# Performance work log

Hardware: AMD Instinct MI355X
Metric: run time of the kernel (lower is better)

The kernel has to match this reference:

```python
import jax, jax.numpy as jnp
import numpy as np

B, S, D = 1, 2048, 1024
H, HD = 16, 64          # attention heads, head dim (kv_heads = 1 -> MQA)
E, K, FH = 8, 2, 4096   # experts, top-k, expert hidden dim
EPS = 1e-5


def setup_inputs() -> dict:
    key = jax.random.key(0)
    ks = jax.random.split(key, 8)
    std = 0.02
    return {
        "x": jax.random.normal(ks[0], (B, S, D), jnp.float32),
        "Wq": jax.random.normal(ks[1], (D, H * HD), jnp.float32) * std,
        "Wk": jax.random.normal(ks[2], (D, HD), jnp.float32) * std,   # 1 kv head
        "Wv": jax.random.normal(ks[3], (D, HD), jnp.float32) * std,
        "Wo": jax.random.normal(ks[4], (H * HD, D), jnp.float32) * std,
        "g_pre_mqa": jnp.ones((D,), jnp.float32),
        "g_post_mqa": jnp.ones((D,), jnp.float32),
        "g_pre_moe": jnp.ones((D,), jnp.float32),
        "g_post_moe": jnp.ones((D,), jnp.float32),
        "Wr": jax.random.normal(ks[5], (D, E), jnp.float32) * std,
        "W1": jax.random.normal(ks[6], (E, D, FH), jnp.float32) * std,
        "W2": jax.random.normal(ks[7], (E, FH, D), jnp.float32) * std,
    }


def rmsnorm(x, g):
    return x * jax.lax.rsqrt(jnp.mean(x * x, axis=-1, keepdims=True) + EPS) * g


def reference(x, Wq, Wk, Wv, Wo, g_pre_mqa, g_post_mqa, g_pre_moe, g_post_moe, Wr, W1, W2):
    # --- MQA block (inference path, no dropout, no causal mask in source) ---
    h = rmsnorm(x, g_pre_mqa)
    q = (h @ Wq).reshape(B, S, H, HD)
    k = h @ Wk  # [B,S,HD] single kv head, broadcast over H
    v = h @ Wv
    scores = jnp.einsum('bqhd,bkd->bhqk', q, k) / np.float32(np.sqrt(HD))
    probs_attn = jax.nn.softmax(scores, axis=-1)
    attn = jnp.einsum('bhqk,bkd->bqhd', probs_attn, v).reshape(B, S, H * HD) @ Wo
    x = x + rmsnorm(attn, g_post_mqa)

    # --- MoE block: softmax router, top-k sparse combine ---
    h = rmsnorm(x, g_pre_moe)
    logits = h @ Wr                                # [B,S,E]
    routing_probs = jax.nn.softmax(logits, axis=-1)
    _, top_idx = jax.lax.top_k(routing_probs, K)   # [B,S,K]
    mask = jax.nn.one_hot(top_idx, E, dtype=routing_probs.dtype).sum(axis=-2)
    weights = routing_probs * mask                 # zero non-chosen experts
    hid = jax.nn.gelu(jnp.einsum('bsd,edf->bsef', h, W1))   # [B,S,E,FH]
    eout = jnp.einsum('bsef,efd->bsed', hid, W2)            # [B,S,E,D]
    moe_out = jnp.einsum('bsed,bse->bsd', eout, weights)
    x = x + rmsnorm(moe_out, g_post_moe)
    return x, routing_probs
```

## Files before the change

kernel.cpp:

```cpp
#include <hip/hip_runtime.h>

typedef unsigned short u16;

#define DEVFN static __device__ __forceinline__

constexpr int Sq = 2048, Dm = 1024, NH = 16, HDim = 64, NE = 8, FHid = 4096;

typedef __attribute__((ext_vector_type(8))) short bf16x8;
typedef __attribute__((ext_vector_type(4))) float f32x4;

DEVFN float b2f(u16 u) { return __uint_as_float(((unsigned)u) << 16); }
DEVFN u16 f2b(float f) {
  unsigned u = __float_as_uint(f);
  return (u16)((u + 0x7fffu + ((u >> 16) & 1u)) >> 16);
}
DEVFN float gelu_f(float x) {
  float y = 0.7978845608028654f * (x + 0.044715f * x * x * x);
  float t = 1.0f - 2.0f / (__expf(2.0f * y) + 1.0f);
  return 0.5f * x * (1.0f + t);
}

DEVFN void gload16(const u16* g, u16* l) {
  __builtin_amdgcn_global_load_lds((const __attribute__((address_space(1))) void*)g,
                                   (__attribute__((address_space(3))) void*)l, 16, 0, 0);
}

__global__ __launch_bounds__(256) void detect_k(const u16* __restrict__ x, int* __restrict__ flag) {
  int t = threadIdx.x;
  float mx = 0.f;
  for (int i = t; i < 4096; i += 256) mx = fmaxf(mx, fabsf(b2f(x[i])));
#pragma unroll
  for (int m = 32; m; m >>= 1) mx = fmaxf(mx, __shfl_xor(mx, m, 64));
  __shared__ float red[4];
  if ((t & 63) == 0) red[t >> 6] = mx;
  __syncthreads();
  if (t == 0) {
    float m2 = fmaxf(fmaxf(red[0], red[1]), fmaxf(red[2], red[3]));
    flag[0] = (m2 > 1e6f) ? 1 : 0;
  }
}

template <int INM, int RESM>
__global__ __launch_bounds__(64) void rmsnorm2_k(const void* __restrict__ inp, const void* __restrict__ g,
                                                 const void* __restrict__ resp, float* __restrict__ out1,
                                                 const int* __restrict__ dflag) {
  int isf = dflag[0];
  int row = blockIdx.x, t = threadIdx.x;
  long rb = (long)row * Dm;
  float v[16];
#pragma unroll
  for (int j = 0; j < 4; j++) {
    long o = rb + t * 4 + j * 256;
    if (INM == 0 || isf) {
      float4 f = *((const float4*)((const float*)inp + o));
      v[4 * j] = f.x; v[4 * j + 1] = f.y; v[4 * j + 2] = f.z; v[4 * j + 3] = f.w;
    } else {
      ushort4 u = *((const ushort4*)((const u16*)inp + o));
      v[4 * j] = b2f(u.x); v[4 * j + 1] = b2f(u.y); v[4 * j + 2] = b2f(u.z); v[4 * j + 3] = b2f(u.w);
    }
  }
  float ss = 0.f;
#pragma unroll
  for (int j = 0; j < 16; j++) ss += v[j] * v[j];
#pragma unroll
  for (int m = 32; m; m >>= 1) ss += __shfl_xor(ss, m, 64);
  float sc = rsqrtf(ss * (1.0f / Dm) + 1e-5f);
#pragma unroll
  for (int j = 0; j < 4; j++) {
    long o = rb + t * 4 + j * 256;
    int go = t * 4 + j * 256;
    float gf[4];
    if (isf) {
      float4 gv = *((const float4*)((const float*)g + go));
      gf[0] = gv.x; gf[1] = gv.y; gf[2] = gv.z; gf[3] = gv.w;
    } else {
      ushort4 gu = *((const ushort4*)((const u16*)g + go));
      gf[0] = b2f(gu.x); gf[1] = b2f(gu.y); gf[2] = b2f(gu.z); gf[3] = b2f(gu.w);
    }
    float o4[4];
#pragma unroll
    for (int q = 0; q < 4; q++) o4[q] = v[4 * j + q] * sc * gf[q];
    if constexpr (RESM == 1) {
      float4 rf = *((const float4*)((const float*)resp + o));
      o4[0] += rf.x; o4[1] += rf.y; o4[2] += rf.z; o4[3] += rf.w;
    } else if constexpr (RESM == 2) {
      if (isf) {
        float4 rf = *((const float4*)((const float*)resp + o));
        o4[0] += rf.x; o4[1] += rf.y; o4[2] += rf.z; o4[3] += rf.w;
      } else {
        ushort4 ru = *((const ushort4*)((const u16*)resp + o));
        o4[0] += b2f(ru.x); o4[1] += b2f(ru.y); o4[2] += b2f(ru.z); o4[3] += b2f(ru.w);
      }
    }
    float4 of;
    of.x = o4[0]; of.y = o4[1]; of.z = o4[2]; of.w = o4[3];
    *((float4*)(out1 + o)) = of;
  }
}

template <int OP>
__global__ __launch_bounds__(256) void gemm_nn_k(
    const float* __restrict__ A, const void* __restrict__ Braw, long boff,
    float* __restrict__ C, int M, int N, int K,
    const float* __restrict__ wfull, int eidx, const int* __restrict__ dflag) {
  int isf = dflag[0];
  const float* Bf = (const float*)Braw;
  const u16* Bh = (const u16*)Braw;
  int t = threadIdx.x;
  int m0 = blockIdx.y * 64, n0 = blockIdx.x * 64;

  __shared__ float As[64][20];
  __shared__ float Bs[16][68];

  int ty = t >> 4, tx = t & 15;
  float acc[4][4];
#pragma unroll
  for (int i = 0; i < 4; i++)
#pragma unroll
    for (int j = 0; j < 4; j++) acc[i][j] = 0.f;

  for (int k0 = 0; k0 < K; k0 += 16) {
    __syncthreads();
#pragma unroll
    for (int i = 0; i < 4; i++) {
      int idx = t + i * 256;
      int ar = idx >> 4, ac = idx & 15;
      As[ar][ac] = A[(long)(m0 + ar) * K + k0 + ac];
      int br = idx >> 6, bc = idx & 63;
      long bi = boff + (long)(k0 + br) * N + n0 + bc;
      Bs[br][bc] = isf ? Bf[bi] : b2f(Bh[bi]);
    }
    __syncthreads();
#pragma unroll
    for (int kk = 0; kk < 16; kk++) {
      float a[4], b[4];
#pragma unroll
      for (int i = 0; i < 4; i++) a[i] = As[ty * 4 + i][kk];
#pragma unroll
      for (int j = 0; j < 4; j++) b[j] = Bs[kk][tx * 4 + j];
#pragma unroll
      for (int i = 0; i < 4; i++)
#pragma unroll
        for (int j = 0; j < 4; j++) acc[i][j] += a[i] * b[j];
    }
  }
#pragma unroll
  for (int i = 0; i < 4; i++) {
    int row = m0 + ty * 4 + i;
#pragma unroll
    for (int j = 0; j < 4; j++) {
      int col = n0 + tx * 4 + j;
      long cidx = (long)row * N + col;
      float val = acc[i][j];
      if constexpr (OP == 0) C[cidx] = val;
      else if constexpr (OP == 1) C[cidx] = gelu_f(val);
      else C[cidx] += wfull[(long)row * 8 + eidx] * val;
    }
  }
}

__global__ __launch_bounds__(256) void attn_f32_k(
    const float* __restrict__ Qf, const float* __restrict__ Kf, const float* __restrict__ Vf,
    float* __restrict__ Of) {
  int qb = blockIdx.x, h = blockIdx.y;
  int t = threadIdx.x;
  int qr = t >> 2;
  int sub = t & 3;
  __shared__ float Ks[64][68];
  __shared__ float Vs[64][68];
  int qrow = qb * 64 + qr;
  const float* qp = Qf + (long)qrow * Dm + h * HDim + sub * 16;
  float qfr[16];
#pragma unroll
  for (int j = 0; j < 16; j += 4) {
    float4 v = *(const float4*)(qp + j);
    qfr[j] = v.x; qfr[j + 1] = v.y; qfr[j + 2] = v.z; qfr[j + 3] = v.w;
  }
  float o[16];
#pragma unroll
  for (int j = 0; j < 16; j++) o[j] = 0.f;
  float m_i = -3e38f, l_i = 0.f;

  for (int kb = 0; kb < Sq / 64; kb++) {
    __syncthreads();
#pragma unroll
    for (int i = 0; i < 2; i++) {
      int idx = t + i * 256;
      int r = idx >> 3, c8 = (idx & 7) * 8;
      const float* kp = Kf + (long)(kb * 64 + r) * HDim + c8;
      float4 a = *(const float4*)(kp);
      float4 b = *(const float4*)(kp + 4);
      *(float4*)&Ks[r][c8] = a;
      *(float4*)&Ks[r][c8 + 4] = b;
      const float* vp = Vf + (long)(kb * 64 + r) * HDim + c8;
      float4 c = *(const float4*)(vp);
      float4 d = *(const float4*)(vp + 4);
      *(float4*)&Vs[r][c8] = c;
      *(float4*)&Vs[r][c8 + 4] = d;
    }
    __syncthreads();
    float s[64];
#pragma unroll
    for (int j = 0; j < 64; j++) {
      float acc = 0.f;
#pragma unroll
      for (int d = 0; d < 16; d++) acc += qfr[d] * Ks[j][sub * 16 + d];
      s[j] = acc;
    }
#pragma unroll
    for (int j = 0; j < 64; j++) {
      float v = s[j];
      v += __shfl_xor(v, 1, 64);
      v += __shfl_xor(v, 2, 64);
      s[j] = v * 0.125f;
    }
    float mx = s[0];
#pragma unroll
    for (int j = 1; j < 64; j++) mx = fmaxf(mx, s[j]);
    float mn = fmaxf(m_i, mx);
    float alpha = __expf(m_i - mn);
    m_i = mn;
    float ps = 0.f;
#pragma unroll
    for (int j = 0; j < 64; j++) {
      s[j] = __expf(s[j] - mn);
      ps += s[j];
    }
    l_i = l_i * alpha + ps;
#pragma unroll
    for (int d = 0; d < 16; d++) o[d] *= alpha;
#pragma unroll
    for (int j = 0; j < 64; j++)
#pragma unroll
      for (int d = 0; d < 16; d++) o[d] += s[j] * Vs[j][sub * 16 + d];
  }
  float inv = 1.0f / l_i;
#pragma unroll
  for (int d = 0; d < 16; d++)
    Of[(long)qrow * Dm + h * HDim + sub * 16 + d] = o[d] * inv;
}

__global__ __launch_bounds__(256) void router2_k(const float* __restrict__ h2, const void* __restrict__ Wr,
                                                 float* __restrict__ probs_out, float* __restrict__ wfull,
                                                 const int* __restrict__ dflag,
                                                 int* __restrict__ ecnt, int* __restrict__ elist) {
  int isf = dflag[0];
  int tok = blockIdx.x * 256 + threadIdx.x;
  if (tok >= Sq) return;
  const float* hrow = h2 + (long)tok * Dm;
  float acc[8] = {0, 0, 0, 0, 0, 0, 0, 0};
  for (int i = 0; i < Dm; i++) {
    float hv = hrow[i];
    if (isf) {
      const float* wr = (const float*)Wr + (long)i * 8;
#pragma unroll
      for (int e = 0; e < 8; e++) acc[e] += hv * wr[e];
    } else {
      const u16* wr = (const u16*)Wr + (long)i * 8;
#pragma unroll
      for (int e = 0; e < 8; e++) acc[e] += hv * b2f(wr[e]);
    }
  }
  int i1 = 0;
#pragma unroll
  for (int e = 1; e < 8; e++)
    if (acc[e] > acc[i1]) i1 = e;
  int i2 = (i1 == 0) ? 1 : 0;
#pragma unroll
  for (int e = 0; e < 8; e++)
    if (e != i1 && acc[e] > acc[i2]) i2 = e;
  float mx = acc[i1];
  float pr[8], s = 0.f;
#pragma unroll
  for (int e = 0; e < 8; e++) { pr[e] = expf(acc[e] - mx); s += pr[e]; }
  float inv = 1.0f / s;
#pragma unroll
  for (int e = 0; e < 8; e++) {
    float pe = pr[e] * inv;
    probs_out[(long)tok * 8 + e] = pe;
    wfull[(long)tok * 8 + e] = (e == i1 || e == i2) ? pe : 0.f;
  }
  int p1 = atomicAdd(&ecnt[i1], 1);
  elist[i1 * Sq + p1] = tok;
  int p2 = atomicAdd(&ecnt[i2], 1);
  elist[i2 * Sq + p2] = tok;
}

__global__ __launch_bounds__(256) void split_pair_k(const float* __restrict__ in, u16* __restrict__ hi,
                                                    u16* __restrict__ lo, int n4) {
  int i = blockIdx.x * 256 + threadIdx.x;
  if (i >= n4) return;
  float4 v = ((const float4*)in)[i];
  ushort4 h, l;
  h.x = f2b(v.x); l.x = f2b(v.x - b2f(h.x));
  h.y = f2b(v.y); l.y = f2b(v.y - b2f(h.y));
  h.z = f2b(v.z); l.z = f2b(v.z - b2f(h.z));
  h.w = f2b(v.w); l.w = f2b(v.w - b2f(h.w));
  ((ushort4*)hi)[i] = h;
  ((ushort4*)lo)[i] = l;
}

__global__ __launch_bounds__(256) void transpose_bf16_k(const void* __restrict__ B, long boff,
                                                        u16* __restrict__ BT, int K, int N,
                                                        const int* __restrict__ dflag) {
  int isf = dflag[0];
  __shared__ u16 tile[32][33];
  int n0 = blockIdx.x * 32, k0 = blockIdx.y * 32;
  int tx = threadIdx.x & 31, ty = threadIdx.x >> 5;
#pragma unroll
  for (int j = 0; j < 32; j += 8) {
    long idx = boff + (long)(k0 + ty + j) * N + n0 + tx;
    u16 uv = isf ? f2b(((const float*)B)[idx]) : ((const u16*)B)[idx];
    tile[ty + j][tx] = uv;
  }
  __syncthreads();
#pragma unroll
  for (int j = 0; j < 32; j += 8)
    BT[(long)(n0 + ty + j) * K + k0 + tx] = tile[tx][ty + j];
}

__global__ __launch_bounds__(256) void moe_w1_k(
    const u16* __restrict__ Ah, const u16* __restrict__ Al, const u16* __restrict__ BT,
    u16* __restrict__ Ch, u16* __restrict__ Cl, const float* __restrict__ wfull,
    const int* __restrict__ elist, const int* __restrict__ ecnt, int eidx) {
  constexpr int N = FHid, K = Dm;
  int cnt = ecnt[eidx];
  int m0 = blockIdx.y * 128, n0 = blockIdx.x * 128;
  if (m0 >= cnt) return;
  __shared__ __align__(16) u16 sAh[128 * 32];
  __shared__ __align__(16) u16 sAl[128 * 32];
  __shared__ __align__(16) u16 sBT[128 * 32];
  __shared__ int sTok[128];
  int t = threadIdx.x;
  if (t < 128) {
    int r = m0 + t;
    sTok[t] = (r < cnt) ? elist[eidx * Sq + r] : elist[eidx * Sq];
  }
  int l = t & 63, w = t >> 6;
  int wm = w >> 1, wn = w & 1;
  int lr = l & 15, lg = l >> 4;

  f32x4 zero = {0.f, 0.f, 0.f, 0.f};
  f32x4 acc[4][4];
#pragma unroll
  for (int i = 0; i < 4; i++)
#pragma unroll
    for (int j = 0; j < 4; j++) acc[i][j] = zero;

  for (int k0 = 0; k0 < K; k0 += 32) {
    __syncthreads();
#pragma unroll
    for (int i = 0; i < 2; i++) {
      int s = i * 256 + t;
      int r = s >> 2, c = s & 3;
      long ao = (long)sTok[r] * K + k0 + c * 8;
      gload16(Ah + ao, sAh + s * 8);
      gload16(Al + ao, sAl + s * 8);
      gload16(BT + (long)(n0 + r) * K + k0 + c * 8, sBT + s * 8);
    }
    __syncthreads();
    bf16x8 fah[4], fal[4], fbb[4];
#pragma unroll
    for (int f = 0; f < 4; f++) {
      int ra = wm * 64 + f * 16 + lr;
      fah[f] = *(const bf16x8*)(sAh + ra * 32 + lg * 8);
      fal[f] = *(const bf16x8*)(sAl + ra * 32 + lg * 8);
      int rb = wn * 64 + f * 16 + lr;
      fbb[f] = *(const bf16x8*)(sBT + rb * 32 + lg * 8);
    }
#pragma unroll
    for (int i = 0; i < 4; i++)
#pragma unroll
      for (int j = 0; j < 4; j++) {
        acc[i][j] = __builtin_amdgcn_mfma_f32_16x16x32_bf16(fah[i], fbb[j], acc[i][j], 0, 0, 0);
        acc[i][j] = __builtin_amdgcn_mfma_f32_16x16x32_bf16(fal[i], fbb[j], acc[i][j], 0, 0, 0);
      }
  }

#pragma unroll
  for (int i = 0; i < 4; i++) {
#pragma unroll
    for (int j = 0; j < 4; j++) {
#pragma unroll
      for (int q = 0; q < 4; q++) {
        int widx = wm * 64 + i * 16 + lg * 4 + q;
        int col = n0 + wn * 64 + j * 16 + lr;
        bool valid = (m0 + widx) < cnt;
        int tok = sTok[widx];
        float gv = valid ? gelu_f(acc[i][j][q]) * wfull[(long)tok * 8 + eidx] : 0.f;
        u16 hh = f2b(gv);
        long idx = (long)(m0 + widx) * N + col;
        Ch[idx] = hh;
        Cl[idx] = f2b(gv - b2f(hh));
      }
    }
  }
}

__global__ __launch_bounds__(256) void moe_w2_k(
    const u16* __restrict__ Ah, const u16* __restrict__ Al, const u16* __restrict__ BT,
    float* __restrict__ C, const int* __restrict__ elist, const int* __restrict__ ecnt, int eidx) {
  constexpr int N = Dm, K = FHid;
  int cnt = ecnt[eidx];
  int m0 = blockIdx.y * 128, n0 = blockIdx.x * 128;
  if (m0 >= cnt) return;
  int kbeg = blockIdx.z * (K / 4), kend = kbeg + K / 4;
  __shared__ __align__(16) u16 sAh[128 * 32];
  __shared__ __align__(16) u16 sAl[128 * 32];
  __shared__ __align__(16) u16 sBT[128 * 32];
  __shared__ int sTok[128];
  int t = threadIdx.x;
  if (t < 128) {
    int r = m0 + t;
    sTok[t] = (r < cnt) ? elist[eidx * Sq + r] : elist[eidx * Sq];
  }
  int l = t & 63, w = t >> 6;
  int wm = w >> 1, wn = w & 1;
  int lr = l & 15, lg = l >> 4;

  f32x4 zero = {0.f, 0.f, 0.f, 0.f};
  f32x4 acc[4][4];
#pragma unroll
  for (int i = 0; i < 4; i++)
#pragma unroll
    for (int j = 0; j < 4; j++) acc[i][j] = zero;

  for (int k0 = kbeg; k0 < kend; k0 += 32) {
    __syncthreads();
#pragma unroll
    for (int i = 0; i < 2; i++) {
      int s = i * 256 + t;
      int r = s >> 2, c = s & 3;
      long ao = (long)(m0 + r) * K + k0 + c * 8;
      gload16(Ah + ao, sAh + s * 8);
      gload16(Al + ao, sAl + s * 8);
      gload16(BT + (long)(n0 + r) * K + k0 + c * 8, sBT + s * 8);
    }
    __syncthreads();
    bf16x8 fah[4], fal[4], fbb[4];
#pragma unroll
    for (int f = 0; f < 4; f++) {
      int ra = wm * 64 + f * 16 + lr;
      fah[f] = *(const bf16x8*)(sAh + ra * 32 + lg * 8);
      fal[f] = *(const bf16x8*)(sAl + ra * 32 + lg * 8);
      int rb = wn * 64 + f * 16 + lr;
      fbb[f] = *(const bf16x8*)(sBT + rb * 32 + lg * 8);
    }
#pragma unroll
    for (int i = 0; i < 4; i++)
#pragma unroll
      for (int j = 0; j < 4; j++) {
        acc[i][j] = __builtin_amdgcn_mfma_f32_16x16x32_bf16(fah[i], fbb[j], acc[i][j], 0, 0, 0);
        acc[i][j] = __builtin_amdgcn_mfma_f32_16x16x32_bf16(fal[i], fbb[j], acc[i][j], 0, 0, 0);
      }
  }

#pragma unroll
  for (int i = 0; i < 4; i++) {
#pragma unroll
    for (int j = 0; j < 4; j++) {
#pragma unroll
      for (int q = 0; q < 4; q++) {
        int widx = wm * 64 + i * 16 + lg * 4 + q;
        int col = n0 + wn * 64 + j * 16 + lr;
        if ((m0 + widx) < cnt) {
          int tok = sTok[widx];
          atomicAdd(&C[(long)tok * N + col], acc[i][j][q]);
        }
      }
    }
  }
}

extern "C" void kernel_launch(void* const* d_in, const int* in_sizes, int n_in,
                              void* d_out, int out_size, void* d_ws, size_t ws_size,
                              hipStream_t stream) {
  (void)in_sizes; (void)n_in;
  const void* x = d_in[0];
  const void* Wq = d_in[1];
  const void* Wk = d_in[2];
  const void* Wv = d_in[3];
  const void* Wo = d_in[4];
  const void* gpre = d_in[5];
  const void* gpost = d_in[6];
  const void* gpm = d_in[7];
  const void* gpo = d_in[8];
  const void* Wr = d_in[9];
  const void* W1 = d_in[10];
  const void* W2 = d_in[11];

  char* ws = (char*)d_ws;
  size_t off = 0;
  auto AL = [&](size_t b) { size_t o = off; off += (b + 255) & ~(size_t)255; return o; };
  const size_t oFlag = AL(16);
  const size_t oWf = AL((size_t)Sq * NE * 4);
  const size_t oHid = AL((size_t)Sq * FHid * 4);
  const size_t oH2 = AL((size_t)Sq * Dm * 4);
  const size_t oX2 = AL((size_t)Sq * Dm * 4);
  const size_t oMoe = AL((size_t)Sq * Dm * 4);
  const size_t oAp = AL((size_t)Sq * Dm * 4);
  const size_t oAt = AL((size_t)Sq * Dm * 4);
  const size_t oVf = AL((size_t)Sq * HDim * 4);
  const size_t oKf = AL((size_t)Sq * HDim * 4);
  const size_t oQf = AL((size_t)Sq * Dm * 4);
  const size_t oH1 = AL((size_t)Sq * Dm * 4);
  if (off > ws_size || out_size != Sq * Dm + Sq * NE) return;

  float* h1f = (float*)(ws + oH1);
  float* qf = (float*)(ws + oQf);
  float* kf = (float*)(ws + oKf);
  float* vf = (float*)(ws + oVf);
  float* attnf = (float*)(ws + oAt);
  float* attnp = (float*)(ws + oAp);
  float* x2 = (float*)(ws + oX2);
  float* h2f = (float*)(ws + oH2);
  float* moe = (float*)(ws + oMoe);
  float* wfull = (float*)(ws + oWf);
  int* dflag = (int*)(ws + oFlag);
  u16* hidh = (u16*)(ws + oHid);
  u16* hidl = hidh + (size_t)Sq * FHid;
  u16* bt1 = (u16*)(ws + oAt);
  u16* bt2 = (u16*)(ws + oAp);
  u16* h2h = (u16*)(ws + oQf);
  u16* h2l = h2h + (size_t)Sq * Dm;
  int* ecnt = (int*)(ws + oVf);
  int* elist = (int*)(ws + oVf + 256);
  float* out_x = (float*)d_out;
  float* out_probs = out_x + (size_t)Sq * Dm;

  detect_k<<<1, 256, 0, stream>>>((const u16*)x, dflag);

  rmsnorm2_k<1, 0><<<Sq, 64, 0, stream>>>(x, gpre, nullptr, h1f, dflag);

  gemm_nn_k<0><<<dim3(Dm / 64, Sq / 64), 256, 0, stream>>>(h1f, Wq, 0, qf, Sq, Dm, Dm, nullptr, 0, dflag);
  gemm_nn_k<0><<<dim3(HDim / 64, Sq / 64), 256, 0, stream>>>(h1f, Wk, 0, kf, Sq, HDim, Dm, nullptr, 0, dflag);
  gemm_nn_k<0><<<dim3(HDim / 64, Sq / 64), 256, 0, stream>>>(h1f, Wv, 0, vf, Sq, HDim, Dm, nullptr, 0, dflag);

  attn_f32_k<<<dim3(Sq / 64, NH), 256, 0, stream>>>(qf, kf, vf, attnf);

  gemm_nn_k<0><<<dim3(Dm / 64, Sq / 64), 256, 0, stream>>>(attnf, Wo, 0, attnp, Sq, Dm, Dm, nullptr, 0, dflag);

  rmsnorm2_k<0, 2><<<Sq, 64, 0, stream>>>(attnp, gpost, x, x2, dflag);
  rmsnorm2_k<0, 0><<<Sq, 64, 0, stream>>>(x2, gpm, nullptr, h2f, dflag);

  hipMemsetAsync(ws + oVf, 0, 32, stream);
  router2_k<<<Sq / 256, 256, 0, stream>>>(h2f, Wr, out_probs, wfull, dflag, ecnt, elist);

  split_pair_k<<<(Sq * Dm / 4 + 255) / 256, 256, 0, stream>>>(h2f, h2h, h2l, Sq * Dm / 4);

  hipMemsetAsync(ws + oMoe, 0, (size_t)Sq * Dm * 4, stream);
  for (int e = 0; e < NE; e++) {
    transpose_bf16_k<<<dim3(FHid / 32, Dm / 32), 256, 0, stream>>>(
        W1, (long)e * Dm * FHid, bt1, Dm, FHid, dflag);
    moe_w1_k<<<dim3(FHid / 128, Sq / 128), 256, 0, stream>>>(
        h2h, h2l, bt1, hidh, hidl, wfull, elist, ecnt, e);
    transpose_bf16_k<<<dim3(Dm / 32, FHid / 32), 256, 0, stream>>>(
        W2, (long)e * FHid * Dm, bt2, FHid, Dm, dflag);
    moe_w2_k<<<dim3(Dm / 128, Sq / 128, 4), 256, 0, stream>>>(
        hidh, hidl, bt2, moe, elist, ecnt, e);
  }

  rmsnorm2_k<0, 1><<<Sq, 64, 0, stream>>>(moe, gpo, x2, out_x, dflag);
}
```

Measured before the change: 2.488 ms.

## Retile projection GEMMs, parallelize router, merge transposes, drop atomics in expert down-proj

```diff
diff --git a/kernel.cpp b/kernel.cpp
--- a/kernel.cpp
+++ b/kernel.cpp
@@ -43,7 +43,8 @@
 template <int INM, int RESM>
 __global__ __launch_bounds__(64) void rmsnorm2_k(const void* __restrict__ inp, const void* __restrict__ g,
                                                  const void* __restrict__ resp, float* __restrict__ out1,
-                                                 const int* __restrict__ dflag) {
+                                                 const int* __restrict__ dflag,
+                                                 const void* __restrict__ inp2) {
   int isf = dflag[0];
   int row = blockIdx.x, t = threadIdx.x;
   long rb = (long)row * Dm;
@@ -51,7 +52,12 @@
 #pragma unroll
   for (int j = 0; j < 4; j++) {
     long o = rb + t * 4 + j * 256;
-    if (INM == 0 || isf) {
+    if constexpr (INM == 2) {
+      float4 f = *((const float4*)((const float*)inp + o));
+      float4 f2 = *((const float4*)((const float*)inp2 + o));
+      v[4 * j] = f.x + f2.x; v[4 * j + 1] = f.y + f2.y;
+      v[4 * j + 2] = f.z + f2.z; v[4 * j + 3] = f.w + f2.w;
+    } else if (INM == 0 || isf) {
       float4 f = *((const float4*)((const float*)inp + o));
       v[4 * j] = f.x; v[4 * j + 1] = f.y; v[4 * j + 2] = f.z; v[4 * j + 3] = f.w;
     } else {
@@ -155,6 +161,65 @@
       if constexpr (OP == 0) C[cidx] = val;
       else if constexpr (OP == 1) C[cidx] = gelu_f(val);
       else C[cidx] += wfull[(long)row * 8 + eidx] * val;
+    }
+  }
+}
+
+__global__ __launch_bounds__(256) void gemm_big_k(
+    const float* __restrict__ A, const void* __restrict__ Braw,
+    float* __restrict__ C, int M, int N, int K, const int* __restrict__ dflag) {
+  int isf = dflag[0];
+  const float* Bf = (const float*)Braw;
+  const u16* Bh = (const u16*)Braw;
+  int t = threadIdx.x;
+  int m0 = blockIdx.y * 128, n0 = blockIdx.x * 64;
+
+  __shared__ float As[128][21];
+  __shared__ float Bs[16][68];
+
+  int ty = t >> 4, tx = t & 15;
+  float acc[8][4];
+#pragma unroll
+  for (int i = 0; i < 8; i++)
+#pragma unroll
+    for (int j = 0; j < 4; j++) acc[i][j] = 0.f;
+
+  for (int k0 = 0; k0 < K; k0 += 16) {
+    __syncthreads();
+#pragma unroll
+    for (int i = 0; i < 8; i++) {
+      int idx = t + i * 256;
+      int ar = idx >> 4, ac = idx & 15;
+      As[ar][ac] = A[(long)(m0 + ar) * K + k0 + ac];
+    }
+#pragma unroll
+    for (int i = 0; i < 4; i++) {
+      int idx = t + i * 256;
+      int br = idx >> 6, bc = idx & 63;
+      long bi = (long)(k0 + br) * N + n0 + bc;
+      Bs[br][bc] = isf ? Bf[bi] : b2f(Bh[bi]);
+    }
+    __syncthreads();
+#pragma unroll
+    for (int kk = 0; kk < 16; kk++) {
+      float a[8], b[4];
+#pragma unroll
+      for (int i = 0; i < 8; i++) a[i] = As[ty * 8 + i][kk];
+#pragma unroll
+      for (int j = 0; j < 4; j++) b[j] = Bs[kk][tx * 4 + j];
+#pragma unroll
+      for (int i = 0; i < 8; i++)
+#pragma unroll
+        for (int j = 0; j < 4; j++) acc[i][j] += a[i] * b[j];
+    }
+  }
+#pragma unroll
+  for (int i = 0; i < 8; i++) {
+    int row = m0 + ty * 8 + i;
+#pragma unroll
+    for (int j = 0; j < 4; j++) {
+      int col = n0 + tx * 4 + j;
+      C[(long)row * N + col] = acc[i][j];
     }
   }
 }
@@ -245,45 +310,57 @@
                                                  const int* __restrict__ dflag,
                                                  int* __restrict__ ecnt, int* __restrict__ elist) {
   int isf = dflag[0];
-  int tok = blockIdx.x * 256 + threadIdx.x;
+  int gid = blockIdx.x * 256 + threadIdx.x;
+  int tok = gid >> 3, e = gid & 7;
   if (tok >= Sq) return;
   const float* hrow = h2 + (long)tok * Dm;
-  float acc[8] = {0, 0, 0, 0, 0, 0, 0, 0};
-  for (int i = 0; i < Dm; i++) {
-    float hv = hrow[i];
-    if (isf) {
-      const float* wr = (const float*)Wr + (long)i * 8;
-#pragma unroll
-      for (int e = 0; e < 8; e++) acc[e] += hv * wr[e];
-    } else {
-      const u16* wr = (const u16*)Wr + (long)i * 8;
-#pragma unroll
-      for (int e = 0; e < 8; e++) acc[e] += hv * b2f(wr[e]);
-    }
-  }
+  float acc = 0.f;
+  if (isf) {
+    const float* wr = (const float*)Wr;
+    for (int i = 0; i < Dm; i += 4) {
+      float4 h4 = *(const float4*)(hrow + i);
+      acc += h4.x * wr[(long)i * 8 + e];
+      acc += h4.y * wr[(long)(i + 1) * 8 + e];
+      acc += h4.z * wr[(long)(i + 2) * 8 + e];
+      acc += h4.w * wr[(long)(i + 3) * 8 + e];
+    }
+  } else {
+    const u16* wr = (const u16*)Wr;
+    for (int i = 0; i < Dm; i += 4) {
+      float4 h4 = *(const float4*)(hrow + i);
+      acc += h4.x * b2f(wr[(long)i * 8 + e]);
+      acc += h4.y * b2f(wr[(long)(i + 1) * 8 + e]);
+      acc += h4.z * b2f(wr[(long)(i + 2) * 8 + e]);
+      acc += h4.w * b2f(wr[(long)(i + 3) * 8 + e]);
+    }
+  }
+  int lane = threadIdx.x & 63;
+  int gbase = lane & ~7;
+  float vals[8];
+#pragma unroll
+  for (int e2 = 0; e2 < 8; e2++) vals[e2] = __shfl(acc, gbase + e2, 64);
   int i1 = 0;
 #pragma unroll
-  for (int e = 1; e < 8; e++)
-    if (acc[e] > acc[i1]) i1 = e;
+  for (int e2 = 1; e2 < 8; e2++)
+    if (vals[e2] > vals[i1]) i1 = e2;
   int i2 = (i1 == 0) ? 1 : 0;
 #pragma unroll
-  for (int e = 0; e < 8; e++)
-    if (e != i1 && acc[e] > acc[i2]) i2 = e;
-  float mx = acc[i1];
+  for (int e2 = 0; e2 < 8; e2++)
+    if (e2 != i1 && vals[e2] > vals[i2]) i2 = e2;
+  float mx = vals[i1];
   float pr[8], s = 0.f;
 #pragma unroll
-  for (int e = 0; e < 8; e++) { pr[e] = expf(acc[e] - mx); s += pr[e]; }
+  for (int e2 = 0; e2 < 8; e2++) { pr[e2] = expf(vals[e2] - mx); s += pr[e2]; }
   float inv = 1.0f / s;
-#pragma unroll
-  for (int e = 0; e < 8; e++) {
-    float pe = pr[e] * inv;
-    probs_out[(long)tok * 8 + e] = pe;
-    wfull[(long)tok * 8 + e] = (e == i1 || e == i2) ? pe : 0.f;
-  }
-  int p1 = atomicAdd(&ecnt[i1], 1);
-  elist[i1 * Sq + p1] = tok;
-  int p2 = atomicAdd(&ecnt[i2], 1);
-  elist[i2 * Sq + p2] = tok;
+  float pe = pr[e] * inv;
+  probs_out[(long)tok * 8 + e] = pe;
+  wfull[(long)tok * 8 + e] = (e == i1 || e == i2) ? pe : 0.f;
+  if (e == 0) {
+    int p1 = atomicAdd(&ecnt[i1], 1);
+    elist[i1 * Sq + p1] = tok;
+    int p2 = atomicAdd(&ecnt[i2], 1);
+    elist[i2 * Sq + p2] = tok;
+  }
 }
 
 __global__ __launch_bounds__(256) void split_pair_k(const float* __restrict__ in, u16* __restrict__ hi,
@@ -300,12 +377,18 @@
   ((ushort4*)lo)[i] = l;
 }
 
-__global__ __launch_bounds__(256) void transpose_bf16_k(const void* __restrict__ B, long boff,
-                                                        u16* __restrict__ BT, int K, int N,
-                                                        const int* __restrict__ dflag) {
+__global__ __launch_bounds__(256) void transpose2_k(const void* __restrict__ W1p, const void* __restrict__ W2p,
+                                                    long boff, u16* __restrict__ bt1, u16* __restrict__ bt2,
+                                                    const int* __restrict__ dflag) {
   int isf = dflag[0];
+  int z = blockIdx.z;
+  const void* B = z ? W2p : W1p;
+  u16* BT = z ? bt2 : bt1;
+  int K = z ? FHid : Dm;
+  int N = z ? Dm : FHid;
+  int n0 = blockIdx.x * 32, k0 = blockIdx.y * 32;
+  if (n0 >= N || k0 >= K) return;
   __shared__ u16 tile[32][33];
-  int n0 = blockIdx.x * 32, k0 = blockIdx.y * 32;
   int tx = threadIdx.x & 31, ty = threadIdx.x >> 5;
 #pragma unroll
   for (int j = 0; j < 32; j += 8) {
@@ -399,15 +482,17 @@
 
 __global__ __launch_bounds__(256) void moe_w2_k(
     const u16* __restrict__ Ah, const u16* __restrict__ Al, const u16* __restrict__ BT,
-    float* __restrict__ C, const int* __restrict__ elist, const int* __restrict__ ecnt, int eidx) {
+    float* __restrict__ C0, float* __restrict__ C1,
+    const int* __restrict__ elist, const int* __restrict__ ecnt, int eidx) {
   constexpr int N = Dm, K = FHid;
   int cnt = ecnt[eidx];
-  int m0 = blockIdx.y * 128, n0 = blockIdx.x * 128;
+  int m0 = blockIdx.y * 128, n0 = blockIdx.x * 64;
   if (m0 >= cnt) return;
-  int kbeg = blockIdx.z * (K / 4), kend = kbeg + K / 4;
+  float* C = blockIdx.z ? C1 : C0;
+  int kbeg = blockIdx.z * (K / 2), kend = kbeg + K / 2;
   __shared__ __align__(16) u16 sAh[128 * 32];
   __shared__ __align__(16) u16 sAl[128 * 32];
-  __shared__ __align__(16) u16 sBT[128 * 32];
+  __shared__ __align__(16) u16 sBT[64 * 32];
   __shared__ int sTok[128];
   int t = threadIdx.x;
   if (t < 128) {
@@ -419,11 +504,11 @@
   int lr = l & 15, lg = l >> 4;
 
   f32x4 zero = {0.f, 0.f, 0.f, 0.f};
-  f32x4 acc[4][4];
+  f32x4 acc[4][2];
 #pragma unroll
   for (int i = 0; i < 4; i++)
 #pragma unroll
-    for (int j = 0; j < 4; j++) acc[i][j] = zero;
+    for (int j = 0; j < 2; j++) acc[i][j] = zero;
 
   for (int k0 = kbeg; k0 < kend; k0 += 32) {
     __syncthreads();
@@ -434,22 +519,28 @@
       long ao = (long)(m0 + r) * K + k0 + c * 8;
       gload16(Ah + ao, sAh + s * 8);
       gload16(Al + ao, sAl + s * 8);
-      gload16(BT + (long)(n0 + r) * K + k0 + c * 8, sBT + s * 8);
-    }
-    __syncthreads();
-    bf16x8 fah[4], fal[4], fbb[4];
+    }
+    {
+      int r = t >> 2, c = t & 3;
+      gload16(BT + (long)(n0 + r) * K + k0 + c * 8, sBT + t * 8);
+    }
+    __syncthreads();
+    bf16x8 fah[4], fal[4], fbb[2];
 #pragma unroll
     for (int f = 0; f < 4; f++) {
       int ra = wm * 64 + f * 16 + lr;
       fah[f] = *(const bf16x8*)(sAh + ra * 32 + lg * 8);
       fal[f] = *(const bf16x8*)(sAl + ra * 32 + lg * 8);
-      int rb = wn * 64 + f * 16 + lr;
-      fbb[f] = *(const bf16x8*)(sBT + rb * 32 + lg * 8);
+    }
+#pragma unroll
+    for (int j = 0; j < 2; j++) {
+      int rb = wn * 32 + j * 16 + lr;
+      fbb[j] = *(const bf16x8*)(sBT + rb * 32 + lg * 8);
     }
 #pragma unroll
     for (int i = 0; i < 4; i++)
 #pragma unroll
-      for (int j = 0; j < 4; j++) {
+      for (int j = 0; j < 2; j++) {
         acc[i][j] = __builtin_amdgcn_mfma_f32_16x16x32_bf16(fah[i], fbb[j], acc[i][j], 0, 0, 0);
         acc[i][j] = __builtin_amdgcn_mfma_f32_16x16x32_bf16(fal[i], fbb[j], acc[i][j], 0, 0, 0);
       }
@@ -458,14 +549,14 @@
 #pragma unroll
   for (int i = 0; i < 4; i++) {
 #pragma unroll
-    for (int j = 0; j < 4; j++) {
+    for (int j = 0; j < 2; j++) {
 #pragma unroll
       for (int q = 0; q < 4; q++) {
         int widx = wm * 64 + i * 16 + lg * 4 + q;
-        int col = n0 + wn * 64 + j * 16 + lr;
+        int col = n0 + wn * 32 + j * 16 + lr;
         if ((m0 + widx) < cnt) {
           int tok = sTok[widx];
-          atomicAdd(&C[(long)tok * N + col], acc[i][j][q]);
+          C[(long)tok * N + col] += acc[i][j][q];
         }
       }
     }
@@ -523,6 +614,7 @@
   u16* bt2 = (u16*)(ws + oAp);
   u16* h2h = (u16*)(ws + oQf);
   u16* h2l = h2h + (size_t)Sq * Dm;
+  float* moe2 = (float*)(ws + oH1);
   int* ecnt = (int*)(ws + oVf);
   int* elist = (int*)(ws + oVf + 256);
   float* out_x = (float*)d_out;
@@ -530,35 +622,34 @@
 
   detect_k<<<1, 256, 0, stream>>>((const u16*)x, dflag);
 
-  rmsnorm2_k<1, 0><<<Sq, 64, 0, stream>>>(x, gpre, nullptr, h1f, dflag);
-
-  gemm_nn_k<0><<<dim3(Dm / 64, Sq / 64), 256, 0, stream>>>(h1f, Wq, 0, qf, Sq, Dm, Dm, nullptr, 0, dflag);
+  rmsnorm2_k<1, 0><<<Sq, 64, 0, stream>>>(x, gpre, nullptr, h1f, dflag, nullptr);
+
+  gemm_big_k<<<dim3(Dm / 64, Sq / 128), 256, 0, stream>>>(h1f, Wq, qf, Sq, Dm, Dm, dflag);
   gemm_nn_k<0><<<dim3(HDim / 64, Sq / 64), 256, 0, stream>>>(h1f, Wk, 0, kf, Sq, HDim, Dm, nullptr, 0, dflag);
   gemm_nn_k<0><<<dim3(HDim / 64, Sq / 64), 256, 0, stream>>>(h1f, Wv, 0, vf, Sq, HDim, Dm, nullptr, 0, dflag);
 
   attn_f32_k<<<dim3(Sq / 64, NH), 256, 0, stream>>>(qf, kf, vf, attnf);
 
-  gemm_nn_k<0><<<dim3(Dm / 64, Sq / 64), 256, 0, stream>>>(attnf, Wo, 0, attnp, Sq, Dm, Dm, nullptr, 0, dflag);
-
-  rmsnorm2_k<0, 2><<<Sq, 64, 0, stream>>>(attnp, gpost, x, x2, dflag);
-  rmsnorm2_k<0, 0><<<Sq, 64, 0, stream>>>(x2, gpm, nullptr, h2f, dflag);
+  gemm_big_k<<<dim3(Dm / 64, Sq / 128), 256, 0, stream>>>(attnf, Wo, attnp, Sq, Dm, Dm, dflag);
+
+  rmsnorm2_k<0, 2><<<Sq, 64, 0, stream>>>(attnp, gpost, x, x2, dflag, nullptr);
+  rmsnorm2_k<0, 0><<<Sq, 64, 0, stream>>>(x2, gpm, nullptr, h2f, dflag, nullptr);
 
   hipMemsetAsync(ws + oVf, 0, 32, stream);
-  router2_k<<<Sq / 256, 256, 0, stream>>>(h2f, Wr, out_probs, wfull, dflag, ecnt, elist);
+  router2_k<<<Sq * NE / 256, 256, 0, stream>>>(h2f, Wr, out_probs, wfull, dflag, ecnt, elist);
 
   split_pair_k<<<(Sq * Dm / 4 + 255) / 256, 256, 0, stream>>>(h2f, h2h, h2l, Sq * Dm / 4);
 
   hipMemsetAsync(ws + oMoe, 0, (size_t)Sq * Dm * 4, stream);
+  hipMemsetAsync(ws + oH1, 0, (size_t)Sq * Dm * 4, stream);
   for (int e = 0; e < NE; e++) {
-    transpose_bf16_k<<<dim3(FHid / 32, Dm / 32), 256, 0, stream>>>(
-        W1, (long)e * Dm * FHid, bt1, Dm, FHid, dflag);
+    transpose2_k<<<dim3(128, 128, 2), 256, 0, stream>>>(
+        W1, W2, (long)e * Dm * FHid, bt1, bt2, dflag);
     moe_w1_k<<<dim3(FHid / 128, Sq / 128), 256, 0, stream>>>(
         h2h, h2l, bt1, hidh, hidl, wfull, elist, ecnt, e);
-    transpose_bf16_k<<<dim3(Dm / 32, FHid / 32), 256, 0, stream>>>(
-        W2, (long)e * FHid * Dm, bt2, FHid, Dm, dflag);
-    moe_w2_k<<<dim3(Dm / 128, Sq / 128, 4), 256, 0, stream>>>(
-        hidh, hidl, bt2, moe, elist, ecnt, e);
-  }
-
-  rmsnorm2_k<0, 1><<<Sq, 64, 0, stream>>>(moe, gpo, x2, out_x, dflag);
-}
+    moe_w2_k<<<dim3(Dm / 64, Sq / 128, 2), 256, 0, stream>>>(
+        hidh, hidl, bt2, moe, moe2, elist, ecnt, e);
+  }
+
+  rmsnorm2_k<2, 1><<<Sq, 64, 0, stream>>>(moe, gpo, x2, out_x, dflag, moe2);
+}
```

New measurement: 2.515 ms. No clear change (+1.1%).
